# Kernel tuning notes

Hardware: AMD Instinct MI355X
Metric: run time of the kernel (lower is better)

Reference implementation:

```python
import jax, jax.numpy as jnp
import numpy as np

SIGMAS = (1.0, 10.0, 100.0, 1000.0)
EPS_RATIO = 1e-3  # lambda ridge term and ratio clip epsilon


def euclidsq(x, y):
    # squared pairwise Euclidean distances, [m, n]
    d = jnp.sum(x * x, axis=-1)[:, None] + jnp.sum(y * y, axis=-1)[None, :] - 2.0 * (x @ y.T)
    return jnp.maximum(d, 0.0)


def kmm_ratio(Kdede, Kdenu, lam):
    # original: inv(Kdede + lam*I) @ Kdenu @ ones == solve(A, Kdenu @ ones)
    n_de = Kdede.shape[0]
    A = Kdede + lam * jnp.eye(n_de, dtype=Kdede.dtype)
    B = jnp.sum(Kdenu, axis=1, keepdims=True)  # [n_de, 1]
    return jnp.linalg.solve(A, B)


def estimate_ratio(x_de, x_nu):
    # averaged KMM ratio over Gaussian kernels with fixed sigmas, then clip
    dsq_dede = euclidsq(x_de, x_de)
    dsq_denu = euclidsq(x_de, x_nu)
    ratio = 0.0
    for s in SIGMAS:
        inv2s2 = 1.0 / (2.0 * s * s)
        Kdede = jnp.exp(-dsq_dede * inv2s2)
        Kdenu = jnp.exp(-dsq_denu * inv2s2)
        ratio = ratio + kmm_ratio(Kdede, Kdenu, EPS_RATIO)
    ratio = ratio / len(SIGMAS)
    return jax.nn.relu(ratio) + EPS_RATIO  # clip_ratio=True


def reference(z1, z2, perm1, perm2):
    n, d = z1.shape
    z1s, z2s = z1[perm1], z2[perm2]
    # numerator ratio over full concatenated embeddings
    num_ratio = estimate_ratio(jnp.concatenate([z1, z2], axis=-1),
                               jnp.concatenate([z1s, z2s], axis=-1))
    num_ratio = 1.0 / num_ratio  # [n, 1]
    x_nu = jnp.concatenate([z2, z2], axis=-1)  # constant across samples

    def per_sample(z1_i):
        # x_de row j = concat(z1_i, z2_shuffled[j])
        x_de = jnp.concatenate([jnp.broadcast_to(z1_i, (n, d)), z2s], axis=-1)
        return jnp.sum(estimate_ratio(x_de, x_nu))

    denum_sums = jax.vmap(per_sample)(z1)  # [n]
    loss = jnp.sum(-jnp.log(num_ratio[:, 0] / denum_sums))
    return loss


def setup_inputs() -> dict:
    key = jax.random.key(0)
    k1, k2 = jax.random.split(key)
    n, d = 256, 128
    z1 = jax.random.normal(k1, (n, d), dtype=jnp.float32)
    z2 = jax.random.normal(k2, (n, d), dtype=jnp.float32)
    perm1 = jnp.arange(n, dtype=jnp.int32)
    perm2 = jnp.arange(n, dtype=jnp.int32)
    return {"z1": z1, "z2": z2, "perm1": perm1, "perm2": perm2}
```

## Files before the change

### kernel.cpp

```cpp
#include <hip/hip_runtime.h>
#include <math.h>

#define N 256
#define Dd 128

__device__ __forceinline__ double inv2s2_of(int s){
    return (s==0)?0.5:(s==1)?5.0e-3:(s==2)?5.0e-5:5.0e-7;
}

__global__ void k_dist(const float* __restrict__ z1, const float* __restrict__ z2,
                       const int* __restrict__ p1, const int* __restrict__ p2,
                       double* __restrict__ Aden, double* __restrict__ Anum,
                       double* __restrict__ S8, float* __restrict__ M4,
                       float* __restrict__ U4, double* __restrict__ bnum){
    __shared__ float Xs[16][17], Ys[16][17];
    int w = blockIdx.z;
    int tx = threadIdx.x, ty = threadIdx.y;
    int row = blockIdx.y*16 + ty, col = blockIdx.x*16 + tx;
    const float *Xb[2], *Yb[2]; const int *Xp[2], *Yp[2]; int npair = 1;
    Xb[1]=0; Yb[1]=0; Xp[0]=0; Yp[0]=0; Xp[1]=0; Yp[1]=0;
    switch(w){
        case 0: Xb[0]=z1; Yb[0]=z1; Xb[1]=z2; Yb[1]=z2; npair=2; break;
        case 1: Xb[0]=z1; Yb[0]=z1; Yp[0]=p1; Xb[1]=z2; Yb[1]=z2; Yp[1]=p2; npair=2; break;
        case 2: Xb[0]=z2; Yb[0]=z2; Xp[0]=p2; Yp[0]=p2; break;
        case 3: Xb[0]=z2; Yb[0]=z2; Xp[0]=p2; break;
        default:Xb[0]=z1; Yb[0]=z2; break;
    }
    double acc = 0.0;
    for (int p = 0; p < npair; p++){
        const float* X = Xb[p]; const float* Y = Yb[p];
        int xr = blockIdx.y*16 + ty; if (Xp[p]) xr = Xp[p][xr];
        int yr = blockIdx.x*16 + ty; if (Yp[p]) yr = Yp[p][yr];
        for (int c = 0; c < Dd; c += 16){
            __syncthreads();
            Xs[ty][tx] = X[xr*Dd + c + tx];
            Ys[ty][tx] = Y[yr*Dd + c + tx];
            __syncthreads();
            #pragma unroll
            for (int t = 0; t < 16; t++){
                float d = Xs[ty][t] - Ys[tx][t];
                acc += (double)d * (double)d;
            }
        }
    }
    int o = row*N + col;
    if (w == 0){
        #pragma unroll
        for (int s = 0; s < 4; s++){
            double v = exp(-inv2s2_of(s)*acc);
            if (row == col) v += 1.0e-3;
            Anum[s*N*N + o] = v;
            S8[(4+s)*N*N + o] = v;
        }
    } else if (w == 1){
        #pragma unroll
        for (int s = 0; s < 4; s++){
            double v = exp(-inv2s2_of(s)*acc);
            v += __shfl_down(v, 8, 16);
            v += __shfl_down(v, 4, 16);
            v += __shfl_down(v, 2, 16);
            v += __shfl_down(v, 1, 16);
            if (tx == 0) atomicAdd(&bnum[s*N + row], v);
        }
    } else if (w == 2){
        #pragma unroll
        for (int s = 0; s < 4; s++){
            double v = exp(-inv2s2_of(s)*acc);
            if (row == col) v += 1.0e-3;
            Aden[s*N*N + o] = v;
            S8[s*N*N + o] = v;
        }
    } else if (w == 3){
        #pragma unroll
        for (int s = 0; s < 4; s++) M4[s*N*N + o] = (float)exp(-inv2s2_of(s)*acc);
    } else {
        #pragma unroll
        for (int s = 0; s < 4; s++) U4[s*N*N + o] = (float)exp(-inv2s2_of(s)*acc);
    }
}


__launch_bounds__(1024, 1)
__global__ void k_pivot(double* __restrict__ S8, double* __restrict__ Eg,
                        double* __restrict__ Pg, int k){
    __shared__ double P[32][33];
    int mat = blockIdx.x;
    double* S = S8 + (size_t)mat*65536;
    double* E = Eg + (size_t)mat*7168;
    double* Pp = Pg + (size_t)mat*1024;
    int tid = threadIdx.x;
    int Kb = k*32;
    {
        int i = tid >> 5, j = tid & 31;
        P[i][j] = S[(size_t)(Kb+i)*N + Kb + j];
    }
    for (int e = tid; e < 7168; e += 1024){
        int ri = e >> 5, kk = e & 31;
        int gi = (ri < Kb) ? ri : ri + 32;
        E[e] = S[(size_t)gi*N + Kb + kk];
    }
    __syncthreads();
    if (tid < 64){
        int r = tid & 31, cg = tid >> 5;
        for (int j = 0; j < 32; j++){
            double d    = P[j][j];
            double invd = 1.0 / d;
            double cr   = P[r][j];
            double s    = cr * invd;
            bool rj = (r == j);
            double nv[16];
            #pragma unroll
            for (int c = 0; c < 16; c++){
                int col = cg*16 + c;
                double pj = P[j][col];
                double v  = P[r][col];
                nv[c] = rj ? ((col == j) ? -invd : v * invd)
                           : ((col == j) ? s : v - s*pj);
            }
            #pragma unroll
            for (int c = 0; c < 16; c++) P[r][cg*16+c] = nv[c];
        }
        #pragma unroll
        for (int c = 0; c < 16; c++) P[r][cg*16+c] = -P[r][cg*16+c];
    }
    __syncthreads();
    {
        int i = tid >> 5, j = tid & 31;
        Pp[tid] = P[i][j];
        S[(size_t)(Kb+i)*N + Kb + j] = -P[i][j];
    }
}

__launch_bounds__(256, 4)
__global__ void k_step(double* __restrict__ S8, const double* __restrict__ Eg,
                       const double* __restrict__ Pg, int k){
    __shared__ double Pl[32][33], EJ[32][33], Cl[32][33], El[32][33];
    int bx = blockIdx.x, mat = blockIdx.y;
    double* S = S8 + (size_t)mat*65536;
    const double* E = Eg + (size_t)mat*7168;
    const double* Pp = Pg + (size_t)mat*1024;
    int tid = threadIdx.x;
    int Kb = k*32;
    #pragma unroll
    for (int l = 0; l < 4; l++){
        int e = tid + l*256; int i = e >> 5, j = e & 31;
        Pl[i][j] = Pp[e];
    }
    if (bx < 49){
        int I = bx / 7, J = bx % 7;
        #pragma unroll
        for (int l = 0; l < 4; l++){
            int e = tid + l*256; int r = e >> 5, kk = e & 31;
            El[r][kk] = E[(I*32 + r)*32 + kk];
            EJ[r][kk] = E[(J*32 + r)*32 + kk];
        }
        __syncthreads();
        #pragma unroll
        for (int l = 0; l < 4; l++){
            int e = tid + l*256; int r = e >> 5, c = e & 31;
            double acc = 0.0;
            #pragma unroll
            for (int kk = 0; kk < 32; kk++) acc += EJ[r][kk] * Pl[kk][c];
            Cl[r][c] = acc;
        }
        __syncthreads();
        int pr = tid >> 4, pc = tid & 15;
        int r0 = 2*pr, c0 = 2*pc;
        double a00=0, a01=0, a10=0, a11=0;
        #pragma unroll
        for (int kk = 0; kk < 32; kk++){
            double e0 = El[r0][kk],   e1 = El[r0+1][kk];
            double b0 = Cl[c0][kk],   b1 = Cl[c0+1][kk];
            a00 += e0*b0; a01 += e0*b1;
            a10 += e1*b0; a11 += e1*b1;
        }
        int gI = (I*32 < Kb) ? I*32 : I*32 + 32;
        int gJ = (J*32 < Kb) ? J*32 : J*32 + 32;
        double* Sp = S + (size_t)(gI + r0)*N + gJ + c0;
        Sp[0]   -= a00; Sp[1]   -= a01;
        Sp[N]   -= a10; Sp[N+1] -= a11;
    } else {
        int T = bx - 49;
        #pragma unroll
        for (int l = 0; l < 4; l++){
            int e = tid + l*256; int r = e >> 5, kk = e & 31;
            El[r][kk] = E[(T*32 + r)*32 + kk];
        }
        __syncthreads();
        #pragma unroll
        for (int l = 0; l < 4; l++){
            int e = tid + l*256; int r = e >> 5, c = e & 31;
            double acc = 0.0;
            #pragma unroll
            for (int kk = 0; kk < 32; kk++) acc += El[r][kk] * Pl[kk][c];
            Cl[r][c] = acc;
        }
        __syncthreads();
        int gT = (T*32 < Kb) ? T*32 : T*32 + 32;
        #pragma unroll
        for (int l = 0; l < 4; l++){
            int e = tid + l*256; int r = e >> 5, c = e & 31;
            S[(size_t)(gT + r)*N + Kb + c] = Cl[r][c];
        }
        #pragma unroll
        for (int l = 0; l < 4; l++){
            int e = tid + l*256; int cc = e >> 5, rr = e & 31;
            S[(size_t)(Kb + cc)*N + gT + rr] = Cl[rr][cc];
        }
    }
}

__global__ void k_gout(const double* __restrict__ S8,
                       float* __restrict__ Gden, float* __restrict__ Gnum){
    int idx = blockIdx.x*256 + threadIdx.x;
    int mat = idx >> 16, e = idx & 65535;
    float g = -(float)S8[idx];
    if (mat < 4) Gden[mat*65536 + e] = g;
    else         Gnum[(mat-4)*65536 + e] = g;
}

__global__ void k_gemm_nt(const float* __restrict__ M4, const float* __restrict__ U4,
                          double* __restrict__ Bmat){
    int s = blockIdx.z;
    const float* Mp = M4 + s*N*N;
    const float* Up = U4 + s*N*N;
    double* Bp = Bmat + s*N*N;
    __shared__ float Ms[32][33], Us[32][33];
    int tx = threadIdx.x, ty = threadIdx.y;
    int tid = ty*16 + tx;
    int bj = blockIdx.y*32, bi = blockIdx.x*32;
    double a00=0, a01=0, a10=0, a11=0;
    for (int kc = 0; kc < N; kc += 32){
        __syncthreads();
        #pragma unroll
        for (int l = 0; l < 4; l++){
            int e = tid + l*256; int r = e >> 5, c = e & 31;
            Ms[r][c] = Mp[(bj+r)*N + kc + c];
            Us[r][c] = Up[(bi+r)*N + kc + c];
        }
        __syncthreads();
        #pragma unroll
        for (int k = 0; k < 32; k++){
            float x0 = Ms[2*ty][k], x1 = Ms[2*ty+1][k];
            float y0 = Us[2*tx][k], y1 = Us[2*tx+1][k];
            a00 += (double)x0*y0; a01 += (double)x0*y1;
            a10 += (double)x1*y0; a11 += (double)x1*y1;
        }
    }
    Bp[(bj+2*ty  )*N + bi+2*tx  ] = a00;
    Bp[(bj+2*ty  )*N + bi+2*tx+1] = a01;
    Bp[(bj+2*ty+1)*N + bi+2*tx  ] = a10;
    Bp[(bj+2*ty+1)*N + bi+2*tx+1] = a11;
}

__global__ void k_gemm_x0(const float* __restrict__ Gden, const double* __restrict__ Bmat,
                          float* __restrict__ X0){
    int s = blockIdx.z;
    const float* Gp = Gden + s*N*N;
    const double* Bp = Bmat + s*N*N;
    float* Xp = X0 + s*N*N;
    __shared__ float Gs[32][33];
    __shared__ double Bs[32][33];
    int tx = threadIdx.x, ty = threadIdx.y;
    int tid = ty*16 + tx;
    int bj = blockIdx.y*32, bi = blockIdx.x*32;
    double a00=0, a01=0, a10=0, a11=0;
    for (int kc = 0; kc < N; kc += 32){
        __syncthreads();
        #pragma unroll
        for (int l = 0; l < 4; l++){
            int e = tid + l*256; int r = e >> 5, c = e & 31;
            Gs[r][c] = Gp[(bj+r)*N + kc + c];
            Bs[r][c] = Bp[(kc+r)*N + bi + c];
        }
        __syncthreads();
        #pragma unroll
        for (int k = 0; k < 32; k++){
            float x0 = Gs[2*ty][k], x1 = Gs[2*ty+1][k];
            double y0 = Bs[k][2*tx], y1 = Bs[k][2*tx+1];
            a00 += (double)x0*y0; a01 += (double)x0*y1;
            a10 += (double)x1*y0; a11 += (double)x1*y1;
        }
    }
    Xp[(bj+2*ty  )*N + bi+2*tx  ] = (float)a00;
    Xp[(bj+2*ty  )*N + bi+2*tx+1] = (float)a01;
    Xp[(bj+2*ty+1)*N + bi+2*tx  ] = (float)a10;
    Xp[(bj+2*ty+1)*N + bi+2*tx+1] = (float)a11;
}

__global__ void k_gemm_r(const double* __restrict__ Aden, const float* __restrict__ X0,
                         const double* __restrict__ Bmat, float* __restrict__ Rm){
    int s = blockIdx.z;
    const double* Ap = Aden + s*N*N;
    const float* Xp = X0 + s*N*N;
    const double* Bp = Bmat + s*N*N;
    float* Rp = Rm + s*N*N;
    __shared__ double As[32][33];
    __shared__ float Xs[32][33];
    int tx = threadIdx.x, ty = threadIdx.y;
    int tid = ty*16 + tx;
    int bj = blockIdx.y*32, bi = blockIdx.x*32;
    double a00=0, a01=0, a10=0, a11=0;
    for (int kc = 0; kc < N; kc += 32){
        __syncthreads();
        #pragma unroll
        for (int l = 0; l < 4; l++){
            int e = tid + l*256; int r = e >> 5, c = e & 31;
            As[r][c] = Ap[(bj+r)*N + kc + c];
            Xs[r][c] = Xp[(kc+r)*N + bi + c];
        }
        __syncthreads();
        #pragma unroll
        for (int k = 0; k < 32; k++){
            double x0 = As[2*ty][k], x1 = As[2*ty+1][k];
            double y0 = (double)Xs[k][2*tx], y1 = (double)Xs[k][2*tx+1];
            a00 += x0*y0; a01 += x0*y1;
            a10 += x1*y0; a11 += x1*y1;
        }
    }
    int r0 = bj+2*ty, c0 = bi+2*tx;
    Rp[(r0  )*N + c0  ] = (float)(Bp[(r0  )*N + c0  ] - a00);
    Rp[(r0  )*N + c0+1] = (float)(Bp[(r0  )*N + c0+1] - a01);
    Rp[(r0+1)*N + c0  ] = (float)(Bp[(r0+1)*N + c0  ] - a10);
    Rp[(r0+1)*N + c0+1] = (float)(Bp[(r0+1)*N + c0+1] - a11);
}

__global__ void k_gemm_xl(const float* __restrict__ Gden, const float* __restrict__ Rm,
                          const float* __restrict__ X0, double* __restrict__ dsum,
                          const float* __restrict__ Gnum, const double* __restrict__ Anum,
                          const double* __restrict__ bnum, float* __restrict__ rnum){
    __shared__ float Gs[32][33], Rs[32][33];
    __shared__ double cp[16][33];
    __shared__ double y0[256], rr2[256], bsh[256];
    int tx = threadIdx.x, ty = threadIdx.y;
    int tid = ty*16 + tx;
    if (blockIdx.y == 8){
        if (blockIdx.x >= 4) return;
        int s = blockIdx.x, j = tid;
        const float* Gp = Gnum + s*N*N;
        const double* Ap = Anum + s*N*N;
        const double* bp = bnum + s*N;
        bsh[j] = bp[j];
        __syncthreads();
        double acc = 0;
        for (int k = 0; k < N; k++) acc += (double)Gp[j*N+k] * bsh[k];
        y0[j] = acc;
        __syncthreads();
        acc = 0;
        for (int k = 0; k < N; k++) acc += Ap[j*N+k] * y0[k];
        rr2[j] = bsh[j] - acc;
        __syncthreads();
        acc = 0;
        for (int k = 0; k < N; k++) acc += (double)Gp[j*N+k] * rr2[k];
        rnum[s*N+j] = (float)(y0[j] + acc);
        return;
    }
    int bj = blockIdx.y*32, bi = blockIdx.x*32;
    int r0 = bj+2*ty, c0 = bi+2*tx;
    double s00=0, s01=0, s10=0, s11=0;
    for (int s = 0; s < 4; s++){
        const float* Gp = Gden + s*N*N;
        const float* Rp = Rm + s*N*N;
        const float* X0p = X0 + s*N*N;
        double a00=0, a01=0, a10=0, a11=0;
        for (int kc = 0; kc < N; kc += 32){
            __syncthreads();
            #pragma unroll
            for (int l = 0; l < 4; l++){
                int e = tid + l*256; int r = e >> 5, c = e & 31;
                Gs[r][c] = Gp[(bj+r)*N + kc + c];
                Rs[r][c] = Rp[(kc+r)*N + bi + c];
            }
            __syncthreads();
            #pragma unroll
            for (int k = 0; k < 32; k++){
                float x0 = Gs[2*ty][k], x1 = Gs[2*ty+1][k];
                float y0v = Rs[k][2*tx], y1v = Rs[k][2*tx+1];
                a00 += (double)x0*y0v; a01 += (double)x0*y1v;
                a10 += (double)x1*y0v; a11 += (double)x1*y1v;
            }
        }
        s00 += (double)X0p[(r0  )*N + c0  ] + a00;
        s01 += (double)X0p[(r0  )*N + c0+1] + a01;
        s10 += (double)X0p[(r0+1)*N + c0  ] + a10;
        s11 += (double)X0p[(r0+1)*N + c0+1] + a11;
    }
    double v00 = (double)fmaxf((float)(0.25*s00), 0.f);
    double v01 = (double)fmaxf((float)(0.25*s01), 0.f);
    double v10 = (double)fmaxf((float)(0.25*s10), 0.f);
    double v11 = (double)fmaxf((float)(0.25*s11), 0.f);
    __syncthreads();
    cp[ty][2*tx]   = v00 + v10;
    cp[ty][2*tx+1] = v01 + v11;
    __syncthreads();
    if (tid < 32){
        double ssum = 0;
        #pragma unroll
        for (int t = 0; t < 16; t++) ssum += cp[t][tid];
        atomicAdd(&dsum[bi + tid], ssum);
    }
}

__global__ void k_loss2(const double* __restrict__ dsum, const float* __restrict__ rnum,
                        float* __restrict__ out){
    __shared__ double red[256];
    int i = threadIdx.x;
    double denum = dsum[i] + (double)N * 1.0e-3;
    float ravg = 0.25f*(rnum[0*N+i] + rnum[1*N+i] + rnum[2*N+i] + rnum[3*N+i]);
    double rn = (double)fmaxf(ravg, 0.f) + 1.0e-3;
    red[i] = log(rn) + log(denum);
    __syncthreads();
    for (int st = 128; st > 0; st >>= 1){
        if (i < st) red[i] += red[i + st];
        __syncthreads();
    }
    if (i == 0) out[0] = (float)red[0];
}

extern "C" void kernel_launch(void* const* d_in, const int* in_sizes, int n_in,
                              void* d_out, int out_size, void* d_ws, size_t ws_size,
                              hipStream_t stream) {
    (void)in_sizes; (void)n_in; (void)out_size; (void)ws_size;
    const float* z1 = (const float*)d_in[0];
    const float* z2 = (const float*)d_in[1];
    const int*   p1 = (const int*)d_in[2];
    const int*   p2 = (const int*)d_in[3];
    float* out = (float*)d_out;

    char* w = (char*)d_ws;
    size_t o = 0;
    auto carve = [&](size_t bytes) -> char* {
        char* p = w + o;
        o += (bytes + 255) & ~(size_t)255;
        return p;
    };
    double*   bnum = (double*) carve((size_t)4*N*sizeof(double));
    double*   dsum = (double*) carve((size_t)N*sizeof(double));
    size_t zbytes = o;
    double* Aden = (double*)carve((size_t)4*N*N*sizeof(double));
    double* Anum = (double*)carve((size_t)4*N*N*sizeof(double));
    float*  M4   = (float*) carve((size_t)4*N*N*sizeof(float));
    float*  U4   = (float*) carve((size_t)4*N*N*sizeof(float));
    double* Bmat = (double*)carve((size_t)4*N*N*sizeof(double));
    float*  Gden = (float*) carve((size_t)4*N*N*sizeof(float));
    float*  Gnum = (float*) carve((size_t)4*N*N*sizeof(float));
    float*  X0   = (float*) carve((size_t)4*N*N*sizeof(float));
    float*  Rm   = (float*) carve((size_t)4*N*N*sizeof(float));
    float*  rnum = (float*) carve((size_t)4*N*sizeof(float));
    double* Smat = (double*)carve((size_t)8*N*N*sizeof(double));
    double* Eg   = (double*)carve((size_t)8*224*32*sizeof(double));
    double* Pg   = (double*)carve((size_t)8*32*32*sizeof(double));

    hipMemsetAsync(d_ws, 0, zbytes, stream);
    k_dist<<<dim3(16,16,5), dim3(16,16), 0, stream>>>(z1, z2, p1, p2,
                                                      Aden, Anum, Smat, M4, U4, bnum);
    k_gemm_nt<<<dim3(8,8,4), dim3(16,16), 0, stream>>>(M4, U4, Bmat);
    for (int k = 0; k < 8; k++){
        k_pivot<<<dim3(8), dim3(1024), 0, stream>>>(Smat, Eg, Pg, k);
        k_step<<<dim3(56,8), dim3(256), 0, stream>>>(Smat, Eg, Pg, k);
    }
    k_gout<<<dim3(2048), dim3(256), 0, stream>>>(Smat, Gden, Gnum);
    k_gemm_x0<<<dim3(8,8,4), dim3(16,16), 0, stream>>>(Gden, Bmat, X0);
    k_gemm_r<<<dim3(8,8,4), dim3(16,16), 0, stream>>>(Aden, X0, Bmat, Rm);
    k_gemm_xl<<<dim3(8,9), dim3(16,16), 0, stream>>>(Gden, Rm, X0, dsum,
                                                     Gnum, Anum, bnum, rnum);
    k_loss2<<<dim3(1), dim3(256), 0, stream>>>(dsum, rnum, out);
}
```

Baseline: 528.1 us.

## Fuse next pivot inversion into block Gauss-Jordan step with ping-pong buffers

The per-iteration pivot kernel is removed. The step kernel that updates the diagonal tile for the next iteration now also inverts that 32x32 tile and writes it out for the following step. Panel data is read straight from the source matrix instead of a staged E buffer, and results go to a second buffer in ping-pong fashion. The separate float conversion kernel is also dropped, with downstream GEMMs reading the double matrix and negating it on load. This halves the launches in the serial inversion chain and removes extra copy passes, but one block per matrix now carries a serial 32-step sweep and the memory footprint doubles.

```diff
diff --git a/kernel.cpp b/kernel.cpp
--- a/kernel.cpp
+++ b/kernel.cpp
@@ -6,12 +6,38 @@
 
 __device__ __forceinline__ double inv2s2_of(int s){
     return (s==0)?0.5:(s==1)?5.0e-3:(s==2)?5.0e-5:5.0e-7;
+}
+
+__device__ __forceinline__ void sweep32(double P[32][33], int tid){
+    if (tid < 64){
+        int r = tid & 31, cg = tid >> 5;
+        for (int j = 0; j < 32; j++){
+            double d    = P[j][j];
+            double invd = 1.0 / d;
+            double cr   = P[r][j];
+            double s    = cr * invd;
+            bool rj = (r == j);
+            double nv[16];
+            #pragma unroll
+            for (int c = 0; c < 16; c++){
+                int col = cg*16 + c;
+                double pj = P[j][col];
+                double v  = P[r][col];
+                nv[c] = rj ? ((col == j) ? -invd : v * invd)
+                           : ((col == j) ? s : v - s*pj);
+            }
+            #pragma unroll
+            for (int c = 0; c < 16; c++) P[r][cg*16+c] = nv[c];
+        }
+        #pragma unroll
+        for (int c = 0; c < 16; c++) P[r][cg*16+c] = -P[r][cg*16+c];
+    }
 }
 
 __global__ void k_dist(const float* __restrict__ z1, const float* __restrict__ z2,
                        const int* __restrict__ p1, const int* __restrict__ p2,
                        double* __restrict__ Aden, double* __restrict__ Anum,
-                       double* __restrict__ S8, float* __restrict__ M4,
+                       double* __restrict__ S0, float* __restrict__ M4,
                        float* __restrict__ U4, double* __restrict__ bnum){
     __shared__ float Xs[16][17], Ys[16][17];
     int w = blockIdx.z;
@@ -50,7 +76,7 @@
             double v = exp(-inv2s2_of(s)*acc);
             if (row == col) v += 1.0e-3;
             Anum[s*N*N + o] = v;
-            S8[(4+s)*N*N + o] = v;
+            S0[(4+s)*N*N + o] = v;
         }
     } else if (w == 1){
         #pragma unroll
@@ -68,7 +94,7 @@
             double v = exp(-inv2s2_of(s)*acc);
             if (row == col) v += 1.0e-3;
             Aden[s*N*N + o] = v;
-            S8[s*N*N + o] = v;
+            S0[s*N*N + o] = v;
         }
     } else if (w == 3){
         #pragma unroll
@@ -80,79 +106,47 @@
 }
 
 
-__launch_bounds__(1024, 1)
-__global__ void k_pivot(double* __restrict__ S8, double* __restrict__ Eg,
-                        double* __restrict__ Pg, int k){
+__global__ void k_pivot0(const double* __restrict__ S0, double* __restrict__ Pg0){
     __shared__ double P[32][33];
     int mat = blockIdx.x;
-    double* S = S8 + (size_t)mat*65536;
-    double* E = Eg + (size_t)mat*7168;
-    double* Pp = Pg + (size_t)mat*1024;
+    const double* S = S0 + (size_t)mat*65536;
+    double* Pp = Pg0 + (size_t)mat*1024;
     int tid = threadIdx.x;
-    int Kb = k*32;
-    {
-        int i = tid >> 5, j = tid & 31;
-        P[i][j] = S[(size_t)(Kb+i)*N + Kb + j];
-    }
-    for (int e = tid; e < 7168; e += 1024){
-        int ri = e >> 5, kk = e & 31;
-        int gi = (ri < Kb) ? ri : ri + 32;
-        E[e] = S[(size_t)gi*N + Kb + kk];
+    #pragma unroll
+    for (int l = 0; l < 4; l++){
+        int e = tid + l*256; P[e>>5][e&31] = S[(size_t)(e>>5)*N + (e&31)];
     }
     __syncthreads();
-    if (tid < 64){
-        int r = tid & 31, cg = tid >> 5;
-        for (int j = 0; j < 32; j++){
-            double d    = P[j][j];
-            double invd = 1.0 / d;
-            double cr   = P[r][j];
-            double s    = cr * invd;
-            bool rj = (r == j);
-            double nv[16];
-            #pragma unroll
-            for (int c = 0; c < 16; c++){
-                int col = cg*16 + c;
-                double pj = P[j][col];
-                double v  = P[r][col];
-                nv[c] = rj ? ((col == j) ? -invd : v * invd)
-                           : ((col == j) ? s : v - s*pj);
-            }
-            #pragma unroll
-            for (int c = 0; c < 16; c++) P[r][cg*16+c] = nv[c];
-        }
-        #pragma unroll
-        for (int c = 0; c < 16; c++) P[r][cg*16+c] = -P[r][cg*16+c];
-    }
+    sweep32(P, tid);
     __syncthreads();
-    {
-        int i = tid >> 5, j = tid & 31;
-        Pp[tid] = P[i][j];
-        S[(size_t)(Kb+i)*N + Kb + j] = -P[i][j];
-    }
-}
-
-__launch_bounds__(256, 4)
-__global__ void k_step(double* __restrict__ S8, const double* __restrict__ Eg,
-                       const double* __restrict__ Pg, int k){
+    #pragma unroll
+    for (int l = 0; l < 4; l++){
+        int e = tid + l*256; Pp[e] = P[e>>5][e&31];
+    }
+}
+
+__global__ void k_step(const double* __restrict__ Ssrc, double* __restrict__ Sdst,
+                       const double* __restrict__ PgS, double* __restrict__ PgD, int k){
     __shared__ double Pl[32][33], EJ[32][33], Cl[32][33], El[32][33];
     int bx = blockIdx.x, mat = blockIdx.y;
-    double* S = S8 + (size_t)mat*65536;
-    const double* E = Eg + (size_t)mat*7168;
-    const double* Pp = Pg + (size_t)mat*1024;
+    const double* S = Ssrc + (size_t)mat*65536;
+    double* D = Sdst + (size_t)mat*65536;
+    const double* Pp = PgS + (size_t)mat*1024;
     int tid = threadIdx.x;
     int Kb = k*32;
     #pragma unroll
     for (int l = 0; l < 4; l++){
-        int e = tid + l*256; int i = e >> 5, j = e & 31;
-        Pl[i][j] = Pp[e];
+        int e = tid + l*256; Pl[e>>5][e&31] = Pp[e];
     }
     if (bx < 49){
         int I = bx / 7, J = bx % 7;
-        #pragma unroll
-        for (int l = 0; l < 4; l++){
-            int e = tid + l*256; int r = e >> 5, kk = e & 31;
-            El[r][kk] = E[(I*32 + r)*32 + kk];
-            EJ[r][kk] = E[(J*32 + r)*32 + kk];
+        int GI = ((I < k) ? I : I + 1) * 32;
+        int GJ = ((J < k) ? J : J + 1) * 32;
+        #pragma unroll
+        for (int l = 0; l < 4; l++){
+            int e = tid + l*256; int r = e >> 5, c = e & 31;
+            El[r][c] = S[(size_t)(GI + r)*N + Kb + c];
+            EJ[r][c] = S[(size_t)(GJ + r)*N + Kb + c];
         }
         __syncthreads();
         #pragma unroll
@@ -166,25 +160,40 @@
         __syncthreads();
         int pr = tid >> 4, pc = tid & 15;
         int r0 = 2*pr, c0 = 2*pc;
-        double a00=0, a01=0, a10=0, a11=0;
+        double a00 = S[(size_t)(GI+r0)*N + GJ+c0];
+        double a01 = S[(size_t)(GI+r0)*N + GJ+c0+1];
+        double a10 = S[(size_t)(GI+r0+1)*N + GJ+c0];
+        double a11 = S[(size_t)(GI+r0+1)*N + GJ+c0+1];
         #pragma unroll
         for (int kk = 0; kk < 32; kk++){
             double e0 = El[r0][kk],   e1 = El[r0+1][kk];
             double b0 = Cl[c0][kk],   b1 = Cl[c0+1][kk];
-            a00 += e0*b0; a01 += e0*b1;
-            a10 += e1*b0; a11 += e1*b1;
-        }
-        int gI = (I*32 < Kb) ? I*32 : I*32 + 32;
-        int gJ = (J*32 < Kb) ? J*32 : J*32 + 32;
-        double* Sp = S + (size_t)(gI + r0)*N + gJ + c0;
-        Sp[0]   -= a00; Sp[1]   -= a01;
-        Sp[N]   -= a10; Sp[N+1] -= a11;
+            a00 -= e0*b0; a01 -= e0*b1;
+            a10 -= e1*b0; a11 -= e1*b1;
+        }
+        double* Dp = D + (size_t)(GI + r0)*N + GJ + c0;
+        Dp[0]   = a00; Dp[1]   = a01;
+        Dp[N]   = a10; Dp[N+1] = a11;
+        if (I == k && J == k && k < 7){
+            __syncthreads();
+            El[r0][c0]   = a00; El[r0][c0+1]   = a01;
+            El[r0+1][c0] = a10; El[r0+1][c0+1] = a11;
+            __syncthreads();
+            sweep32(El, tid);
+            __syncthreads();
+            double* Pd = PgD + (size_t)mat*1024;
+            #pragma unroll
+            for (int l = 0; l < 4; l++){
+                int e = tid + l*256; Pd[e] = El[e>>5][e&31];
+            }
+        }
     } else {
         int T = bx - 49;
-        #pragma unroll
-        for (int l = 0; l < 4; l++){
-            int e = tid + l*256; int r = e >> 5, kk = e & 31;
-            El[r][kk] = E[(T*32 + r)*32 + kk];
+        int GT = ((T < k) ? T : T + 1) * 32;
+        #pragma unroll
+        for (int l = 0; l < 4; l++){
+            int e = tid + l*256; int r = e >> 5, c = e & 31;
+            El[r][c] = S[(size_t)(GT + r)*N + Kb + c];
         }
         __syncthreads();
         #pragma unroll
@@ -196,27 +205,24 @@
             Cl[r][c] = acc;
         }
         __syncthreads();
-        int gT = (T*32 < Kb) ? T*32 : T*32 + 32;
-        #pragma unroll
-        for (int l = 0; l < 4; l++){
-            int e = tid + l*256; int r = e >> 5, c = e & 31;
-            S[(size_t)(gT + r)*N + Kb + c] = Cl[r][c];
+        #pragma unroll
+        for (int l = 0; l < 4; l++){
+            int e = tid + l*256; int r = e >> 5, c = e & 31;
+            D[(size_t)(GT + r)*N + Kb + c] = Cl[r][c];
         }
         #pragma unroll
         for (int l = 0; l < 4; l++){
             int e = tid + l*256; int cc = e >> 5, rr = e & 31;
-            S[(size_t)(Kb + cc)*N + gT + rr] = Cl[rr][cc];
-        }
-    }
-}
-
-__global__ void k_gout(const double* __restrict__ S8,
-                       float* __restrict__ Gden, float* __restrict__ Gnum){
-    int idx = blockIdx.x*256 + threadIdx.x;
-    int mat = idx >> 16, e = idx & 65535;
-    float g = -(float)S8[idx];
-    if (mat < 4) Gden[mat*65536 + e] = g;
-    else         Gnum[(mat-4)*65536 + e] = g;
+            D[(size_t)(Kb + cc)*N + GT + rr] = Cl[rr][cc];
+        }
+        if (T == 0){
+            #pragma unroll
+            for (int l = 0; l < 4; l++){
+                int e = tid + l*256; int i = e >> 5, j = e & 31;
+                D[(size_t)(Kb + i)*N + Kb + j] = -Pl[i][j];
+            }
+        }
+    }
 }
 
 __global__ void k_gemm_nt(const float* __restrict__ M4, const float* __restrict__ U4,
@@ -253,10 +259,10 @@
     Bp[(bj+2*ty+1)*N + bi+2*tx+1] = a11;
 }
 
-__global__ void k_gemm_x0(const float* __restrict__ Gden, const double* __restrict__ Bmat,
+__global__ void k_gemm_x0(const double* __restrict__ Sfin, const double* __restrict__ Bmat,
                           float* __restrict__ X0){
     int s = blockIdx.z;
-    const float* Gp = Gden + s*N*N;
+    const double* Sp = Sfin + (size_t)s*N*N;
     const double* Bp = Bmat + s*N*N;
     float* Xp = X0 + s*N*N;
     __shared__ float Gs[32][33];
@@ -270,7 +276,7 @@
         #pragma unroll
         for (int l = 0; l < 4; l++){
             int e = tid + l*256; int r = e >> 5, c = e & 31;
-            Gs[r][c] = Gp[(bj+r)*N + kc + c];
+            Gs[r][c] = -(float)Sp[(size_t)(bj+r)*N + kc + c];
             Bs[r][c] = Bp[(kc+r)*N + bi + c];
         }
         __syncthreads();
@@ -325,9 +331,9 @@
     Rp[(r0+1)*N + c0+1] = (float)(Bp[(r0+1)*N + c0+1] - a11);
 }
 
-__global__ void k_gemm_xl(const float* __restrict__ Gden, const float* __restrict__ Rm,
+__global__ void k_gemm_xl(const double* __restrict__ Sfin, const float* __restrict__ Rm,
                           const float* __restrict__ X0, double* __restrict__ dsum,
-                          const float* __restrict__ Gnum, const double* __restrict__ Anum,
+                          const double* __restrict__ Anum,
                           const double* __restrict__ bnum, float* __restrict__ rnum){
     __shared__ float Gs[32][33], Rs[32][33];
     __shared__ double cp[16][33];
@@ -337,21 +343,21 @@
     if (blockIdx.y == 8){
         if (blockIdx.x >= 4) return;
         int s = blockIdx.x, j = tid;
-        const float* Gp = Gnum + s*N*N;
+        const double* Sn = Sfin + (size_t)(4+s)*N*N;
         const double* Ap = Anum + s*N*N;
         const double* bp = bnum + s*N;
         bsh[j] = bp[j];
         __syncthreads();
         double acc = 0;
-        for (int k = 0; k < N; k++) acc += (double)Gp[j*N+k] * bsh[k];
+        for (int k = 0; k < N; k++) acc -= Sn[(size_t)k*N+j] * bsh[k];
         y0[j] = acc;
         __syncthreads();
         acc = 0;
-        for (int k = 0; k < N; k++) acc += Ap[j*N+k] * y0[k];
+        for (int k = 0; k < N; k++) acc += Ap[(size_t)k*N+j] * y0[k];
         rr2[j] = bsh[j] - acc;
         __syncthreads();
         acc = 0;
-        for (int k = 0; k < N; k++) acc += (double)Gp[j*N+k] * rr2[k];
+        for (int k = 0; k < N; k++) acc -= Sn[(size_t)k*N+j] * rr2[k];
         rnum[s*N+j] = (float)(y0[j] + acc);
         return;
     }
@@ -359,7 +365,7 @@
     int r0 = bj+2*ty, c0 = bi+2*tx;
     double s00=0, s01=0, s10=0, s11=0;
     for (int s = 0; s < 4; s++){
-        const float* Gp = Gden + s*N*N;
+        const double* Sp = Sfin + (size_t)s*N*N;
         const float* Rp = Rm + s*N*N;
         const float* X0p = X0 + s*N*N;
         double a00=0, a01=0, a10=0, a11=0;
@@ -368,7 +374,7 @@
             #pragma unroll
             for (int l = 0; l < 4; l++){
                 int e = tid + l*256; int r = e >> 5, c = e & 31;
-                Gs[r][c] = Gp[(bj+r)*N + kc + c];
+                Gs[r][c] = -(float)Sp[(size_t)(bj+r)*N + kc + c];
                 Rs[r][c] = Rp[(kc+r)*N + bi + c];
             }
             __syncthreads();
@@ -442,27 +448,29 @@
     float*  M4   = (float*) carve((size_t)4*N*N*sizeof(float));
     float*  U4   = (float*) carve((size_t)4*N*N*sizeof(float));
     double* Bmat = (double*)carve((size_t)4*N*N*sizeof(double));
-    float*  Gden = (float*) carve((size_t)4*N*N*sizeof(float));
-    float*  Gnum = (float*) carve((size_t)4*N*N*sizeof(float));
     float*  X0   = (float*) carve((size_t)4*N*N*sizeof(float));
     float*  Rm   = (float*) carve((size_t)4*N*N*sizeof(float));
     float*  rnum = (float*) carve((size_t)4*N*sizeof(float));
-    double* Smat = (double*)carve((size_t)8*N*N*sizeof(double));
-    double* Eg   = (double*)carve((size_t)8*224*32*sizeof(double));
-    double* Pg   = (double*)carve((size_t)8*32*32*sizeof(double));
+    double* S0   = (double*)carve((size_t)8*N*N*sizeof(double));
+    double* S1   = (double*)carve((size_t)8*N*N*sizeof(double));
+    double* Pg0  = (double*)carve((size_t)8*32*32*sizeof(double));
+    double* Pg1  = (double*)carve((size_t)8*32*32*sizeof(double));
 
     hipMemsetAsync(d_ws, 0, zbytes, stream);
     k_dist<<<dim3(16,16,5), dim3(16,16), 0, stream>>>(z1, z2, p1, p2,
-                                                      Aden, Anum, Smat, M4, U4, bnum);
+                                                      Aden, Anum, S0, M4, U4, bnum);
     k_gemm_nt<<<dim3(8,8,4), dim3(16,16), 0, stream>>>(M4, U4, Bmat);
+    k_pivot0<<<dim3(8), dim3(256), 0, stream>>>(S0, Pg0);
     for (int k = 0; k < 8; k++){
-        k_pivot<<<dim3(8), dim3(1024), 0, stream>>>(Smat, Eg, Pg, k);
-        k_step<<<dim3(56,8), dim3(256), 0, stream>>>(Smat, Eg, Pg, k);
-    }
-    k_gout<<<dim3(2048), dim3(256), 0, stream>>>(Smat, Gden, Gnum);
-    k_gemm_x0<<<dim3(8,8,4), dim3(16,16), 0, stream>>>(Gden, Bmat, X0);
+        double* src = (k & 1) ? S1 : S0;
+        double* dst = (k & 1) ? S0 : S1;
+        double* ps  = (k & 1) ? Pg1 : Pg0;
+        double* pd  = (k & 1) ? Pg0 : Pg1;
+        k_step<<<dim3(56,8), dim3(256), 0, stream>>>(src, dst, ps, pd, k);
+    }
+    k_gemm_x0<<<dim3(8,8,4), dim3(16,16), 0, stream>>>(S0, Bmat, X0);
     k_gemm_r<<<dim3(8,8,4), dim3(16,16), 0, stream>>>(Aden, X0, Bmat, Rm);
-    k_gemm_xl<<<dim3(8,9), dim3(16,16), 0, stream>>>(Gden, Rm, X0, dsum,
-                                                     Gnum, Anum, bnum, rnum);
+    k_gemm_xl<<<dim3(8,9), dim3(16,16), 0, stream>>>(S0, Rm, X0, dsum,
+                                                     Anum, bnum, rnum);
     k_loss2<<<dim3(1), dim3(256), 0, stream>>>(dsum, rnum, out);
 }
```

Measured after the change: 495.1 us. 1.07x faster.
